# Performance work log

Measured on AMD Instinct MI355X. Metric: run time of the kernel, lower is better.

## Reference

```python
import jax, jax.numpy as jnp
import numpy as np

H = 128           # hidden_dim
N = 20000         # num_nucleotides
APN = 22          # atoms per nucleotide
A = N * APN       # total atoms
PHYS = 10         # INVARIANT_PHYSICS_DIM


def setup_inputs() -> dict:
    key = jax.random.key(0)
    ks = jax.random.split(key, 12)
    w = lambda k, shape: jax.random.normal(k, shape, dtype=jnp.float32) * 0.05
    return {
        "physics_x": jax.random.normal(ks[0], (A, PHYS), dtype=jnp.float32),
        "learnable_emb": jax.random.normal(ks[1], (A, H), dtype=jnp.float32),
        "atom_to_nuc": (jnp.arange(A) // APN).astype(jnp.int32),  # sorted, every segment non-empty
        "sugar_x": jax.random.normal(ks[2], (N, 8), dtype=jnp.float32),
        "phos_x": jax.random.normal(ks[3], (N, 8), dtype=jnp.float32),
        "num_nucleotides": N,
        # parameters (stored [in, out]; same math as torch Linear)
        "sugar_W": w(ks[4], (8, H)), "sugar_b": jnp.zeros((H,), jnp.float32),
        "phos_W": w(ks[5], (8, H)), "phos_b": jnp.zeros((H,), jnp.float32),
        "attn_W1": w(ks[6], (PHYS + H, H)), "attn_b1": jnp.zeros((H,), jnp.float32),
        "attn_W2": w(ks[7], (H, 1)), "attn_b2": jnp.zeros((1,), jnp.float32),
        "comb_W": w(ks[8], (3 * H, H)), "comb_b": jnp.zeros((H,), jnp.float32),
        "ln_g": jnp.ones((H,), jnp.float32), "ln_b": jnp.zeros((H,), jnp.float32),
        "rot_W1": w(ks[9], (H, H)), "rot_b1": jnp.zeros((H,), jnp.float32),
        "rot_W2": jnp.zeros((H, 4), jnp.float32), "rot_b2": jnp.array([1.0, 0.0, 0.0, 0.0], jnp.float32),
        "tr_W1": w(ks[10], (H, H)), "tr_b1": jnp.zeros((H,), jnp.float32),
        "tr_W2": jnp.zeros((H, 3), jnp.float32), "tr_b2": jnp.zeros((3,), jnp.float32),
    }


def reference(physics_x, learnable_emb, atom_to_nuc, sugar_x, phos_x, num_nucleotides,
              sugar_W, sugar_b, phos_W, phos_b, attn_W1, attn_b1, attn_W2, attn_b2,
              comb_W, comb_b, ln_g, ln_b, rot_W1, rot_b1, rot_W2, rot_b2,
              tr_W1, tr_b1, tr_W2, tr_b2):
    h_sugar = sugar_x @ sugar_W + sugar_b            # [N, H]
    h_phos = phos_x @ phos_W + phos_b                # [N, H]

    full = jnp.concatenate([physics_x, learnable_emb], axis=-1)  # [A, PHYS+H]
    s = (jnp.tanh(full @ attn_W1 + attn_b1) @ attn_W2 + attn_b2)[:, 0]  # [A] attention logits

    # segment softmax over atoms of each nucleotide (replaces the per-nuc Python loop)
    m = jax.ops.segment_max(s, atom_to_nuc, num_segments=num_nucleotides, indices_are_sorted=True)
    e = jnp.exp(s - m[atom_to_nuc])
    den = jax.ops.segment_sum(e, atom_to_nuc, num_segments=num_nucleotides, indices_are_sorted=True)
    w = e / den[atom_to_nuc]                          # [A]
    pooled = jax.ops.segment_sum(w[:, None] * learnable_emb, atom_to_nuc,
                                 num_segments=num_nucleotides, indices_are_sorted=True)  # [N, H]

    z = jnp.concatenate([pooled, h_sugar, h_phos], axis=-1) @ comb_W + comb_b  # [N, H]
    mu = z.mean(axis=-1, keepdims=True)
    var = z.var(axis=-1, keepdims=True)
    zn = (z - mu) / jnp.sqrt(var + 1e-5) * ln_g + ln_b
    nuc_emb = zn * jax.nn.sigmoid(zn)                 # SiLU

    q = jax.nn.silu(nuc_emb @ rot_W1 + rot_b1) @ rot_W2 + rot_b2  # [N, 4]
    quaternions = q / jnp.maximum(jnp.linalg.norm(q, axis=-1, keepdims=True), 1e-12)
    translations = jax.nn.silu(nuc_emb @ tr_W1 + tr_b1) @ tr_W2 + tr_b2  # [N, 3]
    return (quaternions, translations, nuc_emb)
```

## Files before the change

kernel.cpp:

```cpp
#include <hip/hip_runtime.h>

typedef unsigned short u16;
typedef unsigned int   u32;
typedef short bf16x8 __attribute__((ext_vector_type(8)));
typedef float f32x4 __attribute__((ext_vector_type(4)));

#define APN   22
#define NBK   8
#define AB    176
#define EMBS  136
#define PHYSS 32

__device__ __forceinline__ float bflo(u32 u){ return __uint_as_float(u << 16); }
__device__ __forceinline__ float bfhi(u32 u){ return __uint_as_float(u & 0xffff0000u); }
__device__ __forceinline__ u16 f2bf(float f){
  u32 u = __float_as_uint(f);
  u32 r = u + 0x7fffu + ((u >> 16) & 1u);
  return (u16)(r >> 16);
}
__device__ __forceinline__ u32 pack2(float a, float b){
  return (u32)f2bf(a) | ((u32)f2bf(b) << 16);
}
__device__ __forceinline__ float wave_sum(float v){
  #pragma unroll
  for (int off = 32; off; off >>= 1) v += __shfl_xor(v, off, 64);
  return v;
}
__device__ __forceinline__ float fast_tanh(float x){
  float t = __expf(-2.f * x);
  return 2.f * __builtin_amdgcn_rcpf(1.f + t) - 1.f;
}
__device__ __forceinline__ float silu_f(float x){
  return x * __builtin_amdgcn_rcpf(1.f + __expf(-x));
}

__global__ void k_prep_w1(const float* __restrict__ W1, u32* __restrict__ bfrag32)
{
  const int b = blockIdx.x;
  const int ks = b >> 3, t = b & 7;
  const int e0 = threadIdx.x * 2;
  const int lane = e0 >> 3, j = e0 & 7;
  const int n = t * 16 + (lane & 15);
  float v[2];
  #pragma unroll
  for (int i = 0; i < 2; ++i) {
    int kp = ks * 32 + ((lane >> 4) * 8) + j + i;
    float val = 0.f;
    if (kp < 128)       val = W1[(size_t)(10 + kp) * 128 + n];
    else if (kp < 138)  val = W1[(size_t)(kp - 128) * 128 + n];
    v[i] = val;
  }
  bfrag32[((size_t)(b * 64 + lane)) * 4 + (j >> 1)] = pack2(v[0], v[1]);
}

__global__ void k_prep_frag3(const float* __restrict__ combW, const float* __restrict__ rotW1,
                             const float* __restrict__ trW1,
                             u32* __restrict__ combF, u32* __restrict__ rotF, u32* __restrict__ trF)
{
  const int b = blockIdx.x;
  const float* W; u32* outp; int rel;
  if (b < 96)       { W = combW; outp = combF; rel = b; }
  else if (b < 128) { W = rotW1; outp = rotF;  rel = b - 96; }
  else              { W = trW1;  outp = trF;   rel = b - 128; }
  const int ks = rel >> 3, t = rel & 7;
  const int e0 = threadIdx.x * 2;
  const int lane = e0 >> 3, j = e0 & 7;
  const int n = t * 16 + (lane & 15);
  const int k = ks * 32 + ((lane >> 4) * 8) + j;
  outp[((size_t)(rel * 64 + lane)) * 4 + (j >> 1)] =
      pack2(W[(size_t)k * 128 + n], W[(size_t)(k + 1) * 128 + n]);
}

__global__ __launch_bounds__(256, 2) void k_fused(
    const float* __restrict__ phys, const float* __restrict__ emb,
    const float* __restrict__ b1, const float* __restrict__ W2,
    const uint4* __restrict__ bfragG,
    float* __restrict__ pooled, int A, int N)
{
  __shared__ u16 embt[AB][EMBS];
  __shared__ u16 physt[AB][PHYSS];
  __shared__ u16 bfrag[2][8][64][8];
  __shared__ float s_lds[AB];
  __shared__ float w_lds[AB];

  const int tid  = threadIdx.x;
  const int lane = tid & 63;
  const int wv   = tid >> 6;
  const int a0   = blockIdx.x * AB;

  for (int c = tid; c < AB * 32; c += 256) {
    int row = c >> 5, seg = c & 31;
    int ga = a0 + row;
    float4 v = make_float4(0.f, 0.f, 0.f, 0.f);
    if (ga < A) v = *(const float4*)&emb[(size_t)ga * 128 + seg * 4];
    *(uint2*)&embt[row][seg * 4] = make_uint2(pack2(v.x, v.y), pack2(v.z, v.w));
  }
  if (tid < AB) {
    int ga = a0 + tid;
    u32 vals[16];
    #pragma unroll
    for (int i = 0; i < 5; ++i) {
      float2 v = (ga < A) ? *(const float2*)&phys[(size_t)ga * 10 + i * 2] : make_float2(0.f, 0.f);
      vals[i] = pack2(v.x, v.y);
    }
    #pragma unroll
    for (int i = 5; i < 16; ++i) vals[i] = 0u;
    #pragma unroll
    for (int i = 0; i < 4; ++i)
      *(uint4*)&physt[tid][i * 8] = make_uint4(vals[4*i], vals[4*i+1], vals[4*i+2], vals[4*i+3]);
  }
  {
    uint4 p0 = bfragG[tid * 2], p1 = bfragG[tid * 2 + 1];
    ((uint4*)&bfrag[0][0][0][0])[tid * 2]     = p0;
    ((uint4*)&bfrag[0][0][0][0])[tid * 2 + 1] = p1;
  }
  __syncthreads();

  const int mt0  = wv * 3;
  const int mcnt = (wv == 3) ? 2 : 3;
  const int q = lane >> 4, nn = lane & 15;

  f32x4 acc[3][8];
  #pragma unroll
  for (int mi = 0; mi < 3; ++mi)
    #pragma unroll
    for (int t = 0; t < 8; ++t) acc[mi][t] = (f32x4){0.f, 0.f, 0.f, 0.f};

  for (int ks = 0; ks < 5; ++ks) {
    const int buf = ks & 1;
    uint4 p0, p1;
    if (ks < 4) {
      p0 = bfragG[(ks + 1) * 512 + tid * 2];
      p1 = bfragG[(ks + 1) * 512 + tid * 2 + 1];
    }
    bf16x8 af[3];
    #pragma unroll
    for (int mi = 0; mi < 3; ++mi) if (mi < mcnt) {
      int m = (mt0 + mi) * 16 + nn;
      af[mi] = (ks < 4) ? *(const bf16x8*)&embt[m][ks * 32 + q * 8]
                        : *(const bf16x8*)&physt[m][q * 8];
    }
    #pragma unroll
    for (int t = 0; t < 8; ++t) {
      bf16x8 bb = *(const bf16x8*)&bfrag[buf][t][lane][0];
      #pragma unroll
      for (int mi = 0; mi < 3; ++mi) if (mi < mcnt)
        acc[mi][t] = __builtin_amdgcn_mfma_f32_16x16x32_bf16(af[mi], bb, acc[mi][t], 0, 0, 0);
    }
    if (ks < 4) {
      ((uint4*)&bfrag[buf ^ 1][0][0][0])[tid * 2]     = p0;
      ((uint4*)&bfrag[buf ^ 1][0][0][0])[tid * 2 + 1] = p1;
    }
    __syncthreads();
  }

  float b1v[8], w2v[8];
  #pragma unroll
  for (int t = 0; t < 8; ++t) { b1v[t] = b1[t * 16 + nn]; w2v[t] = W2[t * 16 + nn]; }
  #pragma unroll
  for (int mi = 0; mi < 3; ++mi) if (mi < mcnt) {
    float sp[4];
    #pragma unroll
    for (int r = 0; r < 4; ++r) {
      float a = 0.f;
      #pragma unroll
      for (int t = 0; t < 8; ++t) a += fast_tanh(acc[mi][t][r] + b1v[t]) * w2v[t];
      sp[r] = a;
    }
    #pragma unroll
    for (int off = 1; off < 16; off <<= 1)
      #pragma unroll
      for (int r = 0; r < 4; ++r) sp[r] += __shfl_xor(sp[r], off, 64);
    if (nn == 0)
      #pragma unroll
      for (int r = 0; r < 4; ++r) s_lds[(mt0 + mi) * 16 + q * 4 + r] = sp[r];
  }
  __syncthreads();

  {
    int seg = lane >> 5, id = lane & 31;
    int nl = wv * 2 + seg;
    int nuc = blockIdx.x * NBK + nl;
    bool act = (id < APN) && (nuc < N);
    float sv = act ? s_lds[nl * APN + id] : -3.0e38f;
    float mx = sv;
    #pragma unroll
    for (int off = 16; off; off >>= 1) mx = fmaxf(mx, __shfl_xor(mx, off, 32));
    float e = act ? __expf(sv - mx) : 0.f;
    float den = e;
    #pragma unroll
    for (int off = 16; off; off >>= 1) den += __shfl_xor(den, off, 32);
    if (id < APN) w_lds[nl * APN + id] = e / den;
  }
  __syncthreads();

  {
    int nl = tid >> 5, t32 = tid & 31;
    int nuc = blockIdx.x * NBK + nl;
    if (nuc < N) {
      float o0 = 0.f, o1 = 0.f, o2 = 0.f, o3 = 0.f;
      int base = nl * APN;
      #pragma unroll 2
      for (int a = 0; a < APN; ++a) {
        float wa = w_lds[base + a];
        uint2 u = *(const uint2*)&embt[base + a][t32 * 4];
        o0 += wa * bflo(u.x); o1 += wa * bfhi(u.x);
        o2 += wa * bflo(u.y); o3 += wa * bfhi(u.y);
      }
      *(float4*)&pooled[(size_t)nuc * 128 + t32 * 4] = make_float4(o0, o1, o2, o3);
    }
  }
}

__global__ __launch_bounds__(256, 2) void k_combine(
    const float* __restrict__ pooled,
    const float* __restrict__ sugar_x, const float* __restrict__ phos_x,
    const float* __restrict__ sugarW, const float* __restrict__ sugarB,
    const float* __restrict__ phosW, const float* __restrict__ phosB,
    const uint4* __restrict__ combF, const float* __restrict__ combB,
    const float* __restrict__ lng, const float* __restrict__ lnb,
    const uint4* __restrict__ rotF, const float* __restrict__ rotB1,
    const float* __restrict__ rotW2, const float* __restrict__ rotB2,
    const uint4* __restrict__ trF, const float* __restrict__ trB1,
    const float* __restrict__ trW2, const float* __restrict__ trB2,
    float* __restrict__ out, int N)
{
  __shared__ u16 xbuf[64 * 392];
  __shared__ u16 bsl[2][8][64][8];

  const int tid  = threadIdx.x;
  const int lane = tid & 63;
  const int wv   = tid >> 6;
  const int nn   = lane & 15, q = lane >> 4;
  const int nb   = blockIdx.x * 64;
  const size_t t_off  = (size_t)N * 4;
  const size_t ne_off = (size_t)N * 7;

  {
    const int j0 = lane * 2;
    float2 sBv = *(const float2*)&sugarB[j0];
    float2 pBv = *(const float2*)&phosB[j0];
    float2 swv[8], pwv[8];
    #pragma unroll
    for (int k = 0; k < 8; ++k) {
      swv[k] = *(const float2*)&sugarW[(size_t)k * 128 + j0];
      pwv[k] = *(const float2*)&phosW[(size_t)k * 128 + j0];
    }
    #pragma unroll 1
    for (int n = 0; n < 16; ++n) {
      int row = wv * 16 + n, nuc = nb + row;
      u32 up = 0, us = 0, uq = 0;
      if (nuc < N) {
        float2 pl  = ((const float2*)pooled)[(size_t)nuc * 64 + lane];
        float4 sa  = *(const float4*)&sugar_x[(size_t)nuc * 8];
        float4 sb4 = *(const float4*)&sugar_x[(size_t)nuc * 8 + 4];
        float4 pa  = *(const float4*)&phos_x[(size_t)nuc * 8];
        float4 pb4 = *(const float4*)&phos_x[(size_t)nuc * 8 + 4];
        float hs0 = sBv.x + sa.x*swv[0].x + sa.y*swv[1].x + sa.z*swv[2].x + sa.w*swv[3].x
                          + sb4.x*swv[4].x + sb4.y*swv[5].x + sb4.z*swv[6].x + sb4.w*swv[7].x;
        float hs1 = sBv.y + sa.x*swv[0].y + sa.y*swv[1].y + sa.z*swv[2].y + sa.w*swv[3].y
                          + sb4.x*swv[4].y + sb4.y*swv[5].y + sb4.z*swv[6].y + sb4.w*swv[7].y;
        float hp0 = pBv.x + pa.x*pwv[0].x + pa.y*pwv[1].x + pa.z*pwv[2].x + pa.w*pwv[3].x
                          + pb4.x*pwv[4].x + pb4.y*pwv[5].x + pb4.z*pwv[6].x + pb4.w*pwv[7].x;
        float hp1 = pBv.y + pa.x*pwv[0].y + pa.y*pwv[1].y + pa.z*pwv[2].y + pa.w*pwv[3].y
                          + pb4.x*pwv[4].y + pb4.y*pwv[5].y + pb4.z*pwv[6].y + pb4.w*pwv[7].y;
        up = pack2(pl.x, pl.y); us = pack2(hs0, hs1); uq = pack2(hp0, hp1);
      }
      *(u32*)&xbuf[row * 392 +       j0] = up;
      *(u32*)&xbuf[row * 392 + 128 + j0] = us;
      *(u32*)&xbuf[row * 392 + 256 + j0] = uq;
    }
  }
  {
    uint4 p0 = combF[tid * 2], p1 = combF[tid * 2 + 1];
    ((uint4*)&bsl[0][0][0][0])[tid * 2]     = p0;
    ((uint4*)&bsl[0][0][0][0])[tid * 2 + 1] = p1;
  }
  __syncthreads();

  f32x4 acc[8];
  #pragma unroll
  for (int t = 0; t < 8; ++t) acc[t] = (f32x4){0.f, 0.f, 0.f, 0.f};

  const int arow = wv * 16 + nn;
  for (int ks = 0; ks < 12; ++ks) {
    const int buf = ks & 1;
    uint4 n0, n1;
    if (ks < 11) {
      n0 = combF[(ks + 1) * 512 + tid * 2];
      n1 = combF[(ks + 1) * 512 + tid * 2 + 1];
    }
    bf16x8 af = *(const bf16x8*)&xbuf[arow * 392 + ks * 32 + q * 8];
    #pragma unroll
    for (int t = 0; t < 8; ++t) {
      bf16x8 bb = *(const bf16x8*)&bsl[buf][t][lane][0];
      acc[t] = __builtin_amdgcn_mfma_f32_16x16x32_bf16(af, bb, acc[t], 0, 0, 0);
    }
    if (ks < 11) {
      ((uint4*)&bsl[buf ^ 1][0][0][0])[tid * 2]     = n0;
      ((uint4*)&bsl[buf ^ 1][0][0][0])[tid * 2 + 1] = n1;
    }
    __syncthreads();
  }

  {
    float gt[8], bt[8], cbv[8];
    #pragma unroll
    for (int t = 0; t < 8; ++t) {
      gt[t] = lng[t * 16 + nn]; bt[t] = lnb[t * 16 + nn]; cbv[t] = combB[t * 16 + nn];
    }
    #pragma unroll
    for (int r = 0; r < 4; ++r) {
      float z[8]; float s1 = 0.f, s2 = 0.f;
      #pragma unroll
      for (int t = 0; t < 8; ++t) {
        z[t] = acc[t][r] + cbv[t];
        s1 += z[t]; s2 += z[t] * z[t];
      }
      #pragma unroll
      for (int off = 1; off < 16; off <<= 1) {
        s1 += __shfl_xor(s1, off, 64);
        s2 += __shfl_xor(s2, off, 64);
      }
      float mu   = s1 * 0.0078125f;
      float var  = s2 * 0.0078125f - mu * mu;
      float rstd = rsqrtf(var + 1e-5f);
      int row = q * 4 + r, nuc = nb + wv * 16 + row;
      #pragma unroll
      for (int t = 0; t < 8; ++t) {
        float zn = (z[t] - mu) * rstd * gt[t] + bt[t];
        float ne = silu_f(zn);
        if (nuc < N) out[ne_off + (size_t)nuc * 128 + t * 16 + nn] = ne;
        xbuf[(wv * 16 + row) * 136 + t * 16 + nn] = f2bf(ne);
      }
    }
  }
  __syncthreads();

  f32x4 racc[8], tacc[8];
  #pragma unroll
  for (int t = 0; t < 8; ++t) { racc[t] = (f32x4){0.f,0.f,0.f,0.f}; tacc[t] = (f32x4){0.f,0.f,0.f,0.f}; }
  #pragma unroll
  for (int ks = 0; ks < 4; ++ks) {
    bf16x8 af = *(const bf16x8*)&xbuf[arow * 136 + ks * 32 + q * 8];
    #pragma unroll
    for (int t = 0; t < 8; ++t) {
      bf16x8 rb = ((const bf16x8*)rotF)[(ks * 8 + t) * 64 + lane];
      bf16x8 tb = ((const bf16x8*)trF)[(ks * 8 + t) * 64 + lane];
      racc[t] = __builtin_amdgcn_mfma_f32_16x16x32_bf16(af, rb, racc[t], 0, 0, 0);
      tacc[t] = __builtin_amdgcn_mfma_f32_16x16x32_bf16(af, tb, tacc[t], 0, 0, 0);
    }
  }

  {
    float rb1[8], tb1[8], twx[8], twy[8], twz[8]; float4 rw2[8];
    #pragma unroll
    for (int t = 0; t < 8; ++t) {
      int j = t * 16 + nn;
      rb1[t] = rotB1[j]; tb1[t] = trB1[j];
      rw2[t] = *(const float4*)&rotW2[(size_t)j * 4];
      twx[t] = trW2[(size_t)j * 3]; twy[t] = trW2[(size_t)j * 3 + 1]; twz[t] = trW2[(size_t)j * 3 + 2];
    }
    float qb0 = rotB2[0], qb1 = rotB2[1], qb2 = rotB2[2], qb3 = rotB2[3];
    float pb0 = trB2[0], pb1 = trB2[1], pb2 = trB2[2];
    #pragma unroll
    for (int r = 0; r < 4; ++r) {
      float q0=0.f,q1=0.f,q2=0.f,q3=0.f,p0=0.f,p1=0.f,p2=0.f;
      #pragma unroll
      for (int t = 0; t < 8; ++t) {
        float u = silu_f(racc[t][r] + rb1[t]);
        float v = silu_f(tacc[t][r] + tb1[t]);
        q0 += u * rw2[t].x; q1 += u * rw2[t].y; q2 += u * rw2[t].z; q3 += u * rw2[t].w;
        p0 += v * twx[t];   p1 += v * twy[t];   p2 += v * twz[t];
      }
      #pragma unroll
      for (int off = 1; off < 16; off <<= 1) {
        q0 += __shfl_xor(q0, off, 64); q1 += __shfl_xor(q1, off, 64);
        q2 += __shfl_xor(q2, off, 64); q3 += __shfl_xor(q3, off, 64);
        p0 += __shfl_xor(p0, off, 64); p1 += __shfl_xor(p1, off, 64);
        p2 += __shfl_xor(p2, off, 64);
      }
      int nuc = nb + wv * 16 + q * 4 + r;
      if (nn == 0 && nuc < N) {
        q0 += qb0; q1 += qb1; q2 += qb2; q3 += qb3;
        float nrm = fmaxf(sqrtf(q0*q0 + q1*q1 + q2*q2 + q3*q3), 1e-12f);
        float inv = 1.f / nrm;
        out[(size_t)nuc * 4 + 0] = q0 * inv;
        out[(size_t)nuc * 4 + 1] = q1 * inv;
        out[(size_t)nuc * 4 + 2] = q2 * inv;
        out[(size_t)nuc * 4 + 3] = q3 * inv;
        out[t_off + (size_t)nuc * 3 + 0] = p0 + pb0;
        out[t_off + (size_t)nuc * 3 + 1] = p1 + pb1;
        out[t_off + (size_t)nuc * 3 + 2] = p2 + pb2;
      }
    }
  }
}

extern "C" void kernel_launch(void* const* d_in, const int* in_sizes, int n_in,
                              void* d_out, int out_size, void* d_ws, size_t ws_size,
                              hipStream_t stream) {
  const float* phys    = (const float*)d_in[0];
  const float* emb     = (const float*)d_in[1];
  const float* sugar_x = (const float*)d_in[3];
  const float* phos_x  = (const float*)d_in[4];
  const float* sugarW  = (const float*)d_in[6];
  const float* sugarB  = (const float*)d_in[7];
  const float* phosW   = (const float*)d_in[8];
  const float* phosB   = (const float*)d_in[9];
  const float* attnW1  = (const float*)d_in[10];
  const float* attnB1  = (const float*)d_in[11];
  const float* attnW2  = (const float*)d_in[12];
  const float* combW   = (const float*)d_in[14];
  const float* combB   = (const float*)d_in[15];
  const float* lng     = (const float*)d_in[16];
  const float* lnb     = (const float*)d_in[17];
  const float* rotW1   = (const float*)d_in[18];
  const float* rotB1   = (const float*)d_in[19];
  const float* rotW2   = (const float*)d_in[20];
  const float* rotB2   = (const float*)d_in[21];
  const float* trW1    = (const float*)d_in[22];
  const float* trB1    = (const float*)d_in[23];
  const float* trW2    = (const float*)d_in[24];
  const float* trB2    = (const float*)d_in[25];

  const int A = in_sizes[2];
  const int N = in_sizes[3] / 8;

  char* ws = (char*)d_ws;
  u32*   bfragW1 = (u32*)ws;
  u32*   combF   = (u32*)(ws + 40960);
  u32*   rotF    = (u32*)(ws + 139264);
  u32*   trF     = (u32*)(ws + 172032);
  float* pooled  = (float*)(ws + 204800);

  k_prep_w1<<<40, 256, 0, stream>>>(attnW1, bfragW1);
  k_prep_frag3<<<160, 256, 0, stream>>>(combW, rotW1, trW1, combF, rotF, trF);
  k_fused<<<(N + NBK - 1) / NBK, 256, 0, stream>>>(
      phys, emb, attnB1, attnW2, (const uint4*)bfragW1, pooled, A, N);
  k_combine<<<(N + 63) / 64, 256, 0, stream>>>(
      pooled, sugar_x, phos_x, sugarW, sugarB, phosW, phosB,
      (const uint4*)combF, combB, lng, lnb,
      (const uint4*)rotF, rotB1, rotW2, rotB2,
      (const uint4*)trF, trB1, trW2, trB2,
      (float*)d_out, N);
}
```

Before: 446.0 us.

## Split attention GEMM by output columns per wave with register-resident weights

Each wave now owns 32 of the 128 hidden columns and holds its slice of the attention W1 fragments in registers for the whole block. It loops over all 11 row tiles of atoms, so the double-buffered B-fragment staging in LDS and its per-k syncs go away. Physics features are loaded straight from global into A fragments, and embedding staging uses wider 16-byte stores. Partial logits from the four waves are summed in LDS before the softmax. Smaller LDS use allows three blocks per CU, at the cost of an extra cross-lane reduction per row tile and a partial-sum buffer.

```diff
diff --git a/kernel.cpp b/kernel.cpp
--- a/kernel.cpp
+++ b/kernel.cpp
@@ -9,7 +9,6 @@
 #define NBK   8
 #define AB    176
 #define EMBS  136
-#define PHYSS 32
 
 __device__ __forceinline__ float bflo(u32 u){ return __uint_as_float(u << 16); }
 __device__ __forceinline__ float bfhi(u32 u){ return __uint_as_float(u & 0xffff0000u); }
@@ -71,109 +70,83 @@
       pack2(W[(size_t)k * 128 + n], W[(size_t)(k + 1) * 128 + n]);
 }
 
-__global__ __launch_bounds__(256, 2) void k_fused(
+__global__ __launch_bounds__(256, 3) void k_fused(
     const float* __restrict__ phys, const float* __restrict__ emb,
     const float* __restrict__ b1, const float* __restrict__ W2,
     const uint4* __restrict__ bfragG,
     float* __restrict__ pooled, int A, int N)
 {
   __shared__ u16 embt[AB][EMBS];
-  __shared__ u16 physt[AB][PHYSS];
-  __shared__ u16 bfrag[2][8][64][8];
-  __shared__ float s_lds[AB];
+  __shared__ float s_part[4][AB];
   __shared__ float w_lds[AB];
 
   const int tid  = threadIdx.x;
   const int lane = tid & 63;
   const int wv   = tid >> 6;
   const int a0   = blockIdx.x * AB;
-
-  for (int c = tid; c < AB * 32; c += 256) {
-    int row = c >> 5, seg = c & 31;
+  const int q = lane >> 4, nn = lane & 15;
+
+  bf16x8 bb[5][2];
+  #pragma unroll
+  for (int ks = 0; ks < 5; ++ks)
+    #pragma unroll
+    for (int u = 0; u < 2; ++u)
+      bb[ks][u] = ((const bf16x8*)bfragG)[(ks * 8 + wv * 2 + u) * 64 + lane];
+
+  float b1v[2], w2v[2];
+  #pragma unroll
+  for (int u = 0; u < 2; ++u) {
+    int j = (wv * 2 + u) * 16 + nn;
+    b1v[u] = b1[j]; w2v[u] = W2[j];
+  }
+
+  #pragma unroll
+  for (int it = 0; it < (AB * 16) / 256; ++it) {
+    int c = it * 256 + tid;
+    int row = c >> 4, seg = c & 15;
     int ga = a0 + row;
-    float4 v = make_float4(0.f, 0.f, 0.f, 0.f);
-    if (ga < A) v = *(const float4*)&emb[(size_t)ga * 128 + seg * 4];
-    *(uint2*)&embt[row][seg * 4] = make_uint2(pack2(v.x, v.y), pack2(v.z, v.w));
-  }
-  if (tid < AB) {
-    int ga = a0 + tid;
-    u32 vals[16];
-    #pragma unroll
-    for (int i = 0; i < 5; ++i) {
-      float2 v = (ga < A) ? *(const float2*)&phys[(size_t)ga * 10 + i * 2] : make_float2(0.f, 0.f);
-      vals[i] = pack2(v.x, v.y);
-    }
-    #pragma unroll
-    for (int i = 5; i < 16; ++i) vals[i] = 0u;
-    #pragma unroll
-    for (int i = 0; i < 4; ++i)
-      *(uint4*)&physt[tid][i * 8] = make_uint4(vals[4*i], vals[4*i+1], vals[4*i+2], vals[4*i+3]);
-  }
-  {
-    uint4 p0 = bfragG[tid * 2], p1 = bfragG[tid * 2 + 1];
-    ((uint4*)&bfrag[0][0][0][0])[tid * 2]     = p0;
-    ((uint4*)&bfrag[0][0][0][0])[tid * 2 + 1] = p1;
+    float4 v0 = make_float4(0.f, 0.f, 0.f, 0.f), v1 = v0;
+    if (ga < A) {
+      const float4* src = (const float4*)&emb[(size_t)ga * 128 + seg * 8];
+      v0 = src[0]; v1 = src[1];
+    }
+    *(uint4*)&embt[row][seg * 8] =
+        make_uint4(pack2(v0.x, v0.y), pack2(v0.z, v0.w),
+                   pack2(v1.x, v1.y), pack2(v1.z, v1.w));
   }
   __syncthreads();
 
-  const int mt0  = wv * 3;
-  const int mcnt = (wv == 3) ? 2 : 3;
-  const int q = lane >> 4, nn = lane & 15;
-
-  f32x4 acc[3][8];
-  #pragma unroll
-  for (int mi = 0; mi < 3; ++mi)
-    #pragma unroll
-    for (int t = 0; t < 8; ++t) acc[mi][t] = (f32x4){0.f, 0.f, 0.f, 0.f};
-
-  for (int ks = 0; ks < 5; ++ks) {
-    const int buf = ks & 1;
-    uint4 p0, p1;
-    if (ks < 4) {
-      p0 = bfragG[(ks + 1) * 512 + tid * 2];
-      p1 = bfragG[(ks + 1) * 512 + tid * 2 + 1];
-    }
-    bf16x8 af[3];
-    #pragma unroll
-    for (int mi = 0; mi < 3; ++mi) if (mi < mcnt) {
-      int m = (mt0 + mi) * 16 + nn;
-      af[mi] = (ks < 4) ? *(const bf16x8*)&embt[m][ks * 32 + q * 8]
-                        : *(const bf16x8*)&physt[m][q * 8];
-    }
-    #pragma unroll
-    for (int t = 0; t < 8; ++t) {
-      bf16x8 bb = *(const bf16x8*)&bfrag[buf][t][lane][0];
-      #pragma unroll
-      for (int mi = 0; mi < 3; ++mi) if (mi < mcnt)
-        acc[mi][t] = __builtin_amdgcn_mfma_f32_16x16x32_bf16(af[mi], bb, acc[mi][t], 0, 0, 0);
-    }
-    if (ks < 4) {
-      ((uint4*)&bfrag[buf ^ 1][0][0][0])[tid * 2]     = p0;
-      ((uint4*)&bfrag[buf ^ 1][0][0][0])[tid * 2 + 1] = p1;
-    }
-    __syncthreads();
-  }
-
-  float b1v[8], w2v[8];
-  #pragma unroll
-  for (int t = 0; t < 8; ++t) { b1v[t] = b1[t * 16 + nn]; w2v[t] = W2[t * 16 + nn]; }
-  #pragma unroll
-  for (int mi = 0; mi < 3; ++mi) if (mi < mcnt) {
-    float sp[4];
+  #pragma unroll 2
+  for (int tile = 0; tile < 11; ++tile) {
+    const int m  = tile * 16 + nn;
+    const int ga = a0 + m;
+    union { u32 u[4]; bf16x8 v; } apu;
+    #pragma unroll
+    for (int i = 0; i < 4; ++i) {
+      int c = q * 8 + i * 2;
+      float2 pv = make_float2(0.f, 0.f);
+      if (ga < A && c < 10) pv = *(const float2*)&phys[(size_t)ga * 10 + c];
+      apu.u[i] = pack2(pv.x, pv.y);
+    }
+    f32x4 acc0 = (f32x4){0.f, 0.f, 0.f, 0.f};
+    f32x4 acc1 = (f32x4){0.f, 0.f, 0.f, 0.f};
+    #pragma unroll
+    for (int ks = 0; ks < 4; ++ks) {
+      bf16x8 af = *(const bf16x8*)&embt[m][ks * 32 + q * 8];
+      acc0 = __builtin_amdgcn_mfma_f32_16x16x32_bf16(af, bb[ks][0], acc0, 0, 0, 0);
+      acc1 = __builtin_amdgcn_mfma_f32_16x16x32_bf16(af, bb[ks][1], acc1, 0, 0, 0);
+    }
+    acc0 = __builtin_amdgcn_mfma_f32_16x16x32_bf16(apu.v, bb[4][0], acc0, 0, 0, 0);
+    acc1 = __builtin_amdgcn_mfma_f32_16x16x32_bf16(apu.v, bb[4][1], acc1, 0, 0, 0);
+
     #pragma unroll
     for (int r = 0; r < 4; ++r) {
-      float a = 0.f;
-      #pragma unroll
-      for (int t = 0; t < 8; ++t) a += fast_tanh(acc[mi][t][r] + b1v[t]) * w2v[t];
-      sp[r] = a;
-    }
-    #pragma unroll
-    for (int off = 1; off < 16; off <<= 1)
-      #pragma unroll
-      for (int r = 0; r < 4; ++r) sp[r] += __shfl_xor(sp[r], off, 64);
-    if (nn == 0)
-      #pragma unroll
-      for (int r = 0; r < 4; ++r) s_lds[(mt0 + mi) * 16 + q * 4 + r] = sp[r];
+      float a = fast_tanh(acc0[r] + b1v[0]) * w2v[0]
+              + fast_tanh(acc1[r] + b1v[1]) * w2v[1];
+      #pragma unroll
+      for (int off = 1; off < 16; off <<= 1) a += __shfl_xor(a, off, 64);
+      if (nn == 0) s_part[wv][tile * 16 + q * 4 + r] = a;
+    }
   }
   __syncthreads();
 
@@ -182,7 +155,9 @@
     int nl = wv * 2 + seg;
     int nuc = blockIdx.x * NBK + nl;
     bool act = (id < APN) && (nuc < N);
-    float sv = act ? s_lds[nl * APN + id] : -3.0e38f;
+    int idx = nl * APN + id;
+    float sv = act ? (s_part[0][idx] + s_part[1][idx] + s_part[2][idx] + s_part[3][idx])
+                   : -3.0e38f;
     float mx = sv;
     #pragma unroll
     for (int off = 16; off; off >>= 1) mx = fmaxf(mx, __shfl_xor(mx, off, 32));
@@ -190,7 +165,7 @@
     float den = e;
     #pragma unroll
     for (int off = 16; off; off >>= 1) den += __shfl_xor(den, off, 32);
-    if (id < APN) w_lds[nl * APN + id] = e / den;
+    if (id < APN) w_lds[idx] = e / den;
   }
   __syncthreads();
 
```

Result: slower. 456.5 us (+2.3%).
